# Optimization experiments

Measured on AMD Instinct MI355X. Metric: run time of the kernel, lower is better.

The kernel has to match this reference:

```python
import jax, jax.numpy as jnp
import numpy as np

N, F, E = 50000, 128, 800000
H, C1, C2 = 4, 32, 32  # heads, channel_in, channel_out
LRELU_SLOPE = 0.2
LN_EPS = 1e-5


def _gat_conv(x, src, dst, W_src, W_dst, att_src, att_dst, bias, n, h, c):
    # x: [n, f_in]; src/dst: [e] edge endpoints (message j->i)
    xs = (x @ W_src).reshape(n, h, c)  # source-side transform
    xd = (x @ W_dst).reshape(n, h, c)  # dest-side transform
    a_s = jnp.einsum('nhc,hc->nh', xs, att_src)  # [n,h]
    a_d = jnp.einsum('nhc,hc->nh', xd, att_dst)
    e = jax.nn.leaky_relu(a_s[src] + a_d[dst], LRELU_SLOPE)  # [E,h]
    m = jax.lax.stop_gradient(jax.ops.segment_max(e, dst, num_segments=n))
    ee = jnp.exp(e - m[dst])
    denom = jax.ops.segment_sum(ee, dst, num_segments=n)
    alpha = ee / (denom[dst] + 1e-16)  # segment softmax over incoming edges
    out = jax.ops.segment_sum(xs[src] * alpha[:, :, None], dst, num_segments=n)
    return out.reshape(n, h * c) + bias


def _layer_norm(x, gamma, beta):
    mu = jnp.mean(x, axis=-1, keepdims=True)
    var = jnp.var(x, axis=-1, keepdims=True)
    return (x - mu) * jax.lax.rsqrt(var + LN_EPS) * gamma + beta


def setup_inputs() -> dict:
    key = jax.random.key(0)
    ks = jax.random.split(key, 16)
    hid = H * C1  # 128
    out_dim = H * C2  # 128

    def glorot(k, shape, fan_in):
        return jax.random.normal(k, shape, dtype=jnp.float32) / np.sqrt(fan_in)

    x = jax.random.normal(ks[0], (N, F), dtype=jnp.float32)
    edge_index = jax.random.randint(ks[1], (2, E), 0, N, dtype=jnp.int32)

    return {
        'x': x,
        'edge_index': edge_index,
        # conv1 (in F -> H*C1)
        'W1_src': glorot(ks[2], (F, H * C1), F),
        'W1_dst': glorot(ks[3], (F, H * C1), F),
        'att1_src': glorot(ks[4], (H, C1), C1),
        'att1_dst': glorot(ks[5], (H, C1), C1),
        'b1': jnp.zeros((H * C1,), jnp.float32),
        # lin1 skip (F -> hid)
        'Wl1': glorot(ks[6], (F, hid), F),
        'bl1': jnp.zeros((hid,), jnp.float32),
        # LayerNorm over hid
        'gamma': jnp.ones((hid,), jnp.float32),
        'beta': jnp.zeros((hid,), jnp.float32),
        # conv2 (hid -> H*C2)
        'W2_src': glorot(ks[7], (hid, H * C2), hid),
        'W2_dst': glorot(ks[8], (hid, H * C2), hid),
        'att2_src': glorot(ks[9], (H, C2), C2),
        'att2_dst': glorot(ks[10], (H, C2), C2),
        'b2': jnp.zeros((H * C2,), jnp.float32),
        # lin2 skip (hid -> out_dim)
        'Wl2': glorot(ks[11], (hid, out_dim), hid),
        'bl2': jnp.zeros((out_dim,), jnp.float32),
    }


def reference(x, edge_index, W1_src, W1_dst, att1_src, att1_dst, b1, Wl1, bl1,
              gamma, beta, W2_src, W2_dst, att2_src, att2_dst, b2, Wl2, bl2):
    src, dst = edge_index[0], edge_index[1]
    h = _gat_conv(x, src, dst, W1_src, W1_dst, att1_src, att1_dst, b1, N, H, C1) \
        + (x @ Wl1 + bl1)
    h = jax.nn.relu(_layer_norm(h, gamma, beta))
    out = _gat_conv(h, src, dst, W2_src, W2_dst, att2_src, att2_dst, b2, N, H, C2) \
        + (h @ Wl2 + bl2)
    return out
```

## Files before the change

### kernel.cpp

```cpp
#include <hip/hip_runtime.h>

#define N_NODES 50000
#define E_EDGES 800000
#define LRELU 0.2f
#define LN_EPS 1e-5f
#define NBUCK 196
#define BSHIFT 8
#define BCAP 4608

typedef short bf16x8 __attribute__((ext_vector_type(8)));
typedef float f32x4 __attribute__((ext_vector_type(4)));

__device__ __forceinline__ ushort f2bf(float f) {
    uint u = __float_as_uint(f);
    u += 0x7FFF + ((u >> 16) & 1);
    return (ushort)(u >> 16);
}
__device__ __forceinline__ float bflo(uint u) { return __uint_as_float(u << 16); }
__device__ __forceinline__ float bfhi(uint u) { return __uint_as_float(u & 0xFFFF0000u); }

__global__ __launch_bounds__(256) void bucket_scatter_kernel(
    const int* __restrict__ src, const int* __restrict__ dst,
    int* __restrict__ bucketCursor, uint* __restrict__ pairs, int e)
{
    __shared__ int lhist[256];
    __shared__ int lscan[NBUCK];
    __shared__ int lcur[NBUCK];
    __shared__ int lbase[NBUCK];
    __shared__ uint stageW[4096];
    __shared__ int  stageA[4096];
    int t = threadIdx.x;
    int e0 = blockIdx.x * 4096;
    int count = min(4096, e - e0);

    lhist[t] = 0;
    if (t < NBUCK) lcur[t] = 0;
    __syncthreads();

    int  bb[16];
    uint pk[16];
    #pragma unroll
    for (int q = 0; q < 16; ++q) {
        int li = t + q * 256;
        if (li < count) {
            int d = dst[e0 + li];
            int s = src[e0 + li];
            bb[q] = d >> BSHIFT;
            pk[q] = (uint)s | ((uint)(d & 255) << 16);
            atomicAdd(&lhist[bb[q]], 1);
        } else bb[q] = -1;
    }
    __syncthreads();

    int orig = lhist[t];
    #pragma unroll
    for (int off = 1; off < 256; off <<= 1) {
        int u = (t >= off) ? lhist[t - off] : 0;
        __syncthreads();
        lhist[t] += u;
        __syncthreads();
    }
    if (t < NBUCK) {
        lscan[t] = lhist[t] - orig;
        lbase[t] = t * BCAP + (orig ? atomicAdd(&bucketCursor[t], orig) : 0);
    }
    __syncthreads();

    #pragma unroll
    for (int q = 0; q < 16; ++q) {
        if (bb[q] >= 0) {
            int slot = lscan[bb[q]] + atomicAdd(&lcur[bb[q]], 1);
            stageW[slot] = pk[q];
            stageA[slot] = lbase[bb[q]] + (slot - lscan[bb[q]]);
        }
    }
    __syncthreads();

    #pragma unroll
    for (int q = 0; q < 16; ++q) {
        int li = t + q * 256;
        if (li < count) pairs[stageA[li]] = stageW[li];
    }
}

__global__ __launch_bounds__(256) void bucket_sort_kernel(
    const uint* __restrict__ pairs, const int* __restrict__ bucketCursor,
    int* __restrict__ offs, ushort* __restrict__ degs,
    ushort* __restrict__ srcSorted, int n)
{
    __shared__ int cnt[256], cur[256], ls[256];
    int b = blockIdx.x, t = threadIdx.x;
    int base = b * BCAP;
    int m = bucketCursor[b];
    cnt[t] = 0; cur[t] = 0;
    __syncthreads();
    for (int i = t; i < m; i += 256)
        atomicAdd(&cnt[pairs[base + i] >> 16], 1);
    __syncthreads();
    int orig = cnt[t];
    ls[t] = orig;
    __syncthreads();
    #pragma unroll
    for (int off = 1; off < 256; off <<= 1) {
        int u = (t >= off) ? ls[t - off] : 0;
        __syncthreads();
        ls[t] += u;
        __syncthreads();
    }
    int excl = ls[t] - orig;
    int node = (b << BSHIFT) + t;
    if (node < n) {
        offs[node] = base + excl;
        degs[node] = (ushort)orig;
    }
    cnt[t] = excl;
    __syncthreads();
    for (int i = t; i < m; i += 256) {
        uint w = pairs[base + i];
        int dl = w >> 16;
        int pos = cnt[dl] + atomicAdd(&cur[dl], 1);
        srcSorted[base + pos] = (ushort)(w & 0xFFFFu);
    }
}

__global__ __launch_bounds__(256) void prep_all_kernel(
    const float* __restrict__ W1s, const float* __restrict__ Wl1,
    const float* __restrict__ W1d, const float* __restrict__ a1s,
    const float* __restrict__ a1d,
    const float* __restrict__ W2s, const float* __restrict__ Wl2,
    const float* __restrict__ W2d, const float* __restrict__ a2s,
    const float* __restrict__ a2d,
    ushort* __restrict__ Wt, ushort* __restrict__ Watt,
    int* __restrict__ bucketCursor)
{
    int t = threadIdx.x;
    if (blockIdx.x < 256) {
        int idx = blockIdx.x * 256 + t;
        int lw = idx >> 14, rem = idx & 16383;
        int nn = rem >> 7, k = rem & 127;
        const float* W = (lw == 0) ? W1s : (lw == 1) ? Wl1 : (lw == 2) ? W2s : Wl2;
        Wt[idx] = f2bf(W[k * 128 + nn]);
    } else if (blockIdx.x < 258) {
        int L = blockIdx.x - 256;
        const float* Ws = L ? W2s : W1s;
        const float* Wd = L ? W2d : W1d;
        const float* as = L ? a2s : a1s;
        const float* adv = L ? a2d : a1d;
        #pragma unroll
        for (int q = 0; q < 8; ++q) {
            int e = q * 256 + t;
            int c = e >> 7, f = e & 127;
            float v = 0.f;
            if (c < 8) {
                const float* W  = (c < 4) ? Ws : Wd;
                const float* av = (c < 4) ? as : adv;
                int h = c & 3;
                #pragma unroll
                for (int j = 0; j < 32; ++j)
                    v += W[f * 128 + h * 32 + j] * av[h * 32 + j];
            }
            Watt[L * 2048 + c * 128 + f] = f2bf(v);
        }
    } else {
        if (t < NBUCK) bucketCursor[t] = 0;
    }
}

template <int LAYER>
__global__ __launch_bounds__(256) void gemm_fused_kernel(
    const float* __restrict__ Afp, const ushort* __restrict__ Abf,
    const ushort* __restrict__ Wt, const ushort* __restrict__ Watt,
    ushort* __restrict__ Cbf, float* __restrict__ a_sd, int n)
{
    __shared__ ushort Asb[64][136];
    __shared__ ushort Wsb[128][136];
    __shared__ ushort Attb[16][136];
    const int z = blockIdx.x;
    const int row0 = blockIdx.y * 64;
    const int tid = threadIdx.x;

    if (LAYER == 0) {
        #pragma unroll
        for (int i = 0; i < 8; ++i) {
            int idx = tid + i * 256;
            int r = idx >> 5, c4 = idx & 31;
            int grow = row0 + r;
            float4 v = make_float4(0.f, 0.f, 0.f, 0.f);
            if (grow < n) v = *(const float4*)(Afp + (size_t)grow * 128 + c4 * 4);
            ushort4 o;
            o.x = f2bf(v.x); o.y = f2bf(v.y); o.z = f2bf(v.z); o.w = f2bf(v.w);
            *(ushort4*)&Asb[r][c4 * 4] = o;
        }
    } else {
        #pragma unroll
        for (int i = 0; i < 4; ++i) {
            int c = tid + i * 256;
            int r = c >> 4, o = c & 15;
            int grow = row0 + r;
            uint4 v = make_uint4(0, 0, 0, 0);
            if (grow < n) v = *(const uint4*)(Abf + (size_t)grow * 128 + o * 8);
            *(uint4*)&Asb[r][o * 8] = v;
        }
    }
    {
        const ushort* Wz = Wt + (size_t)(LAYER * 2 + z) * 16384;
        #pragma unroll
        for (int i = 0; i < 8; ++i) {
            int c = tid + i * 256;
            int r = c >> 4, o = c & 15;
            uint4 v = *(const uint4*)(Wz + r * 128 + o * 8);
            *(uint4*)&Wsb[r][o * 8] = v;
        }
    }
    if (z == 0) {
        int r = tid >> 4, o = tid & 15;
        uint4 v = *(const uint4*)(Watt + LAYER * 2048 + r * 128 + o * 8);
        *(uint4*)&Attb[r][o * 8] = v;
    }
    __syncthreads();

    const int w = tid >> 6, lane = tid & 63;
    const int wm = w >> 1, wn = w & 1;
    const int l15 = lane & 15, lg = lane >> 4;
    const bool doAtt = (z == 0) && (wn == 0);

    f32x4 acc[2][4];
    f32x4 accA[2];
    #pragma unroll
    for (int m = 0; m < 2; ++m) {
        accA[m] = (f32x4){0.f, 0.f, 0.f, 0.f};
        #pragma unroll
        for (int j = 0; j < 4; ++j)
            acc[m][j] = (f32x4){0.f, 0.f, 0.f, 0.f};
    }

    #pragma unroll
    for (int ks = 0; ks < 4; ++ks) {
        const int k0 = ks * 32 + 4 * lg;
        bf16x8 af[2], bfr[4];
        #pragma unroll
        for (int m = 0; m < 2; ++m) {
            const ushort* p = &Asb[wm * 32 + m * 16 + l15][k0];
            ushort4 lo = *(const ushort4*)p;
            ushort4 hi = *(const ushort4*)(p + 16);
            bf16x8 a;
            a[0] = (short)lo.x; a[1] = (short)lo.y; a[2] = (short)lo.z; a[3] = (short)lo.w;
            a[4] = (short)hi.x; a[5] = (short)hi.y; a[6] = (short)hi.z; a[7] = (short)hi.w;
            af[m] = a;
        }
        #pragma unroll
        for (int j = 0; j < 4; ++j) {
            const ushort* p = &Wsb[wn * 64 + j * 16 + l15][k0];
            ushort4 lo = *(const ushort4*)p;
            ushort4 hi = *(const ushort4*)(p + 16);
            bf16x8 b;
            b[0] = (short)lo.x; b[1] = (short)lo.y; b[2] = (short)lo.z; b[3] = (short)lo.w;
            b[4] = (short)hi.x; b[5] = (short)hi.y; b[6] = (short)hi.z; b[7] = (short)hi.w;
            bfr[j] = b;
        }
        #pragma unroll
        for (int m = 0; m < 2; ++m)
            #pragma unroll
            for (int j = 0; j < 4; ++j)
                acc[m][j] = __builtin_amdgcn_mfma_f32_16x16x32_bf16(
                    af[m], bfr[j], acc[m][j], 0, 0, 0);
        if (doAtt) {
            const ushort* p = &Attb[l15][k0];
            ushort4 lo = *(const ushort4*)p;
            ushort4 hi = *(const ushort4*)(p + 16);
            bf16x8 b;
            b[0] = (short)lo.x; b[1] = (short)lo.y; b[2] = (short)lo.z; b[3] = (short)lo.w;
            b[4] = (short)hi.x; b[5] = (short)hi.y; b[6] = (short)hi.z; b[7] = (short)hi.w;
            #pragma unroll
            for (int m = 0; m < 2; ++m)
                accA[m] = __builtin_amdgcn_mfma_f32_16x16x32_bf16(
                    af[m], b, accA[m], 0, 0, 0);
        }
    }

    if (doAtt && l15 < 8) {
        #pragma unroll
        for (int m = 0; m < 2; ++m)
            #pragma unroll
            for (int r = 0; r < 4; ++r) {
                int grow = row0 + wm * 32 + m * 16 + lg * 4 + r;
                if (grow < n) a_sd[(size_t)grow * 8 + l15] = accA[m][r];
            }
    }

    __syncthreads();
    ushort (*Cs)[136] = (ushort(*)[136])&Asb[0][0];
    #pragma unroll
    for (int m = 0; m < 2; ++m)
        #pragma unroll
        for (int j = 0; j < 4; ++j)
            #pragma unroll
            for (int r = 0; r < 4; ++r)
                Cs[wm * 32 + m * 16 + lg * 4 + r][wn * 64 + j * 16 + l15] =
                    f2bf(acc[m][j][r]);
    __syncthreads();
    #pragma unroll
    for (int i = 0; i < 4; ++i) {
        int u4 = tid + i * 256;
        int r = u4 >> 4, c8 = u4 & 15;
        int grow = row0 + r;
        if (grow < n) {
            uint4 v = *(const uint4*)&Cs[r][c8 * 8];
            *(uint4*)(Cbf + (size_t)grow * 256 + z * 128 + c8 * 8) = v;
        }
    }
}

template <int MODE>
__global__ __launch_bounds__(256) void aggregate_fused_kernel(
    const ushort* __restrict__ srcSorted, const int* __restrict__ offs,
    const ushort* __restrict__ degs,
    const ushort* __restrict__ bufbf,
    const float* __restrict__ a_sd,
    const float* __restrict__ bias_a, const float* __restrict__ bias_l,
    const float* __restrict__ gamma, const float* __restrict__ beta,
    ushort* __restrict__ hbf, float* __restrict__ out, int n)
{
    int node = (blockIdx.x * blockDim.x + threadIdx.x) >> 6;
    int lane = threadIdx.x & 63;
    if (node >= n) return;
    int beg = offs[node];
    int end = beg + degs[node];
    const int q  = lane & 15;
    const int hh = lane >> 4;
    const int g  = lane & 15;
    const int j  = lane >> 4;
    const int h  = g >> 2;

    float adh = a_sd[(size_t)node * 8 + 4 + hh];

    float acc[8] = {};
    float denp = 0.f;

    for (int t = beg; t < end; t += 16) {
        int idx = t + q;
        int ic = (idx < end) ? idx : (end - 1);
        int s = srcSorted[ic];
        float as = a_sd[(size_t)s * 8 + hh];
        float e = as + adh;
        e = (e > 0.f) ? e : LRELU * e;
        float ee = (idx < end) ? __expf(e) : 0.f;
        denp += ee;

        int   sA  = __shfl(s, j);
        int   sB  = __shfl(s, j + 4);
        int   sC  = __shfl(s, j + 8);
        int   sD  = __shfl(s, j + 12);
        float eeA = __shfl(ee, h * 16 + j);
        float eeB = __shfl(ee, h * 16 + j + 4);
        float eeC = __shfl(ee, h * 16 + j + 8);
        float eeD = __shfl(ee, h * 16 + j + 12);
        uint4 xA = *(const uint4*)(bufbf + (size_t)sA * 256 + g * 8);
        uint4 xB = *(const uint4*)(bufbf + (size_t)sB * 256 + g * 8);
        uint4 xC = *(const uint4*)(bufbf + (size_t)sC * 256 + g * 8);
        uint4 xD = *(const uint4*)(bufbf + (size_t)sD * 256 + g * 8);
        acc[0] = fmaf(eeA, bflo(xA.x), acc[0]);
        acc[1] = fmaf(eeA, bfhi(xA.x), acc[1]);
        acc[2] = fmaf(eeA, bflo(xA.y), acc[2]);
        acc[3] = fmaf(eeA, bfhi(xA.y), acc[3]);
        acc[4] = fmaf(eeA, bflo(xA.z), acc[4]);
        acc[5] = fmaf(eeA, bfhi(xA.z), acc[5]);
        acc[6] = fmaf(eeA, bflo(xA.w), acc[6]);
        acc[7] = fmaf(eeA, bfhi(xA.w), acc[7]);
        acc[0] = fmaf(eeB, bflo(xB.x), acc[0]);
        acc[1] = fmaf(eeB, bfhi(xB.x), acc[1]);
        acc[2] = fmaf(eeB, bflo(xB.y), acc[2]);
        acc[3] = fmaf(eeB, bfhi(xB.y), acc[3]);
        acc[4] = fmaf(eeB, bflo(xB.z), acc[4]);
        acc[5] = fmaf(eeB, bfhi(xB.z), acc[5]);
        acc[6] = fmaf(eeB, bflo(xB.w), acc[6]);
        acc[7] = fmaf(eeB, bfhi(xB.w), acc[7]);
        acc[0] = fmaf(eeC, bflo(xC.x), acc[0]);
        acc[1] = fmaf(eeC, bfhi(xC.x), acc[1]);
        acc[2] = fmaf(eeC, bflo(xC.y), acc[2]);
        acc[3] = fmaf(eeC, bfhi(xC.y), acc[3]);
        acc[4] = fmaf(eeC, bflo(xC.z), acc[4]);
        acc[5] = fmaf(eeC, bfhi(xC.z), acc[5]);
        acc[6] = fmaf(eeC, bflo(xC.w), acc[6]);
        acc[7] = fmaf(eeC, bfhi(xC.w), acc[7]);
        acc[0] = fmaf(eeD, bflo(xD.x), acc[0]);
        acc[1] = fmaf(eeD, bfhi(xD.x), acc[1]);
        acc[2] = fmaf(eeD, bflo(xD.y), acc[2]);
        acc[3] = fmaf(eeD, bfhi(xD.y), acc[3]);
        acc[4] = fmaf(eeD, bflo(xD.z), acc[4]);
        acc[5] = fmaf(eeD, bfhi(xD.z), acc[5]);
        acc[6] = fmaf(eeD, bflo(xD.w), acc[6]);
        acc[7] = fmaf(eeD, bfhi(xD.w), acc[7]);
    }

    #pragma unroll
    for (int c = 0; c < 8; ++c) {
        acc[c] += __shfl_xor(acc[c], 16);
        acc[c] += __shfl_xor(acc[c], 32);
    }
    denp += __shfl_xor(denp, 1);
    denp += __shfl_xor(denp, 2);
    denp += __shfl_xor(denp, 4);
    denp += __shfl_xor(denp, 8);
    float den = __shfl(denp, h * 16);

    if (lane < 16) {
        float inv = 1.f / (den + 1e-16f);
        uint4 sk = *(const uint4*)(bufbf + (size_t)node * 256 + 128 + g * 8);
        float4 ba0 = *(const float4*)(bias_a + g * 8);
        float4 ba1 = *(const float4*)(bias_a + g * 8 + 4);
        float4 bl0 = *(const float4*)(bias_l + g * 8);
        float4 bl1 = *(const float4*)(bias_l + g * 8 + 4);
        float v[8];
        v[0] = acc[0] * inv + bflo(sk.x) + ba0.x + bl0.x;
        v[1] = acc[1] * inv + bfhi(sk.x) + ba0.y + bl0.y;
        v[2] = acc[2] * inv + bflo(sk.y) + ba0.z + bl0.z;
        v[3] = acc[3] * inv + bfhi(sk.y) + ba0.w + bl0.w;
        v[4] = acc[4] * inv + bflo(sk.z) + ba1.x + bl1.x;
        v[5] = acc[5] * inv + bfhi(sk.z) + ba1.y + bl1.y;
        v[6] = acc[6] * inv + bflo(sk.w) + ba1.z + bl1.z;
        v[7] = acc[7] * inv + bfhi(sk.w) + ba1.w + bl1.w;

        if (MODE == 0) {
            float sum = 0.f, sq = 0.f;
            #pragma unroll
            for (int c = 0; c < 8; ++c) { sum += v[c]; sq += v[c] * v[c]; }
            #pragma unroll
            for (int off = 1; off < 16; off <<= 1) {
                sum += __shfl_xor(sum, off);
                sq  += __shfl_xor(sq, off);
            }
            float mu = sum * (1.f / 128.f);
            float var = sq * (1.f / 128.f) - mu * mu;
            float rs = rsqrtf(var + LN_EPS);
            float4 gm0 = *(const float4*)(gamma + g * 8);
            float4 gm1 = *(const float4*)(gamma + g * 8 + 4);
            float4 bt0 = *(const float4*)(beta + g * 8);
            float4 bt1 = *(const float4*)(beta + g * 8 + 4);
            float o[8];
            o[0] = fmaxf((v[0] - mu) * rs * gm0.x + bt0.x, 0.f);
            o[1] = fmaxf((v[1] - mu) * rs * gm0.y + bt0.y, 0.f);
            o[2] = fmaxf((v[2] - mu) * rs * gm0.z + bt0.z, 0.f);
            o[3] = fmaxf((v[3] - mu) * rs * gm0.w + bt0.w, 0.f);
            o[4] = fmaxf((v[4] - mu) * rs * gm1.x + bt1.x, 0.f);
            o[5] = fmaxf((v[5] - mu) * rs * gm1.y + bt1.y, 0.f);
            o[6] = fmaxf((v[6] - mu) * rs * gm1.z + bt1.z, 0.f);
            o[7] = fmaxf((v[7] - mu) * rs * gm1.w + bt1.w, 0.f);
            uint4 st;
            st.x = (uint)f2bf(o[0]) | ((uint)f2bf(o[1]) << 16);
            st.y = (uint)f2bf(o[2]) | ((uint)f2bf(o[3]) << 16);
            st.z = (uint)f2bf(o[4]) | ((uint)f2bf(o[5]) << 16);
            st.w = (uint)f2bf(o[6]) | ((uint)f2bf(o[7]) << 16);
            *(uint4*)(hbf + (size_t)node * 128 + g * 8) = st;
        } else {
            *(float4*)(out + (size_t)node * 128 + g * 8) =
                make_float4(v[0], v[1], v[2], v[3]);
            *(float4*)(out + (size_t)node * 128 + g * 8 + 4) =
                make_float4(v[4], v[5], v[6], v[7]);
        }
    }
}

extern "C" void kernel_launch(void* const* d_in, const int* in_sizes, int n_in,
                              void* d_out, int out_size, void* d_ws, size_t ws_size,
                              hipStream_t stream) {
    const float* x       = (const float*)d_in[0];
    const int*   ei      = (const int*)d_in[1];
    const int*   src     = ei;
    const int*   dst     = ei + E_EDGES;
    const float* W1_src  = (const float*)d_in[2];
    const float* W1_dst  = (const float*)d_in[3];
    const float* att1_s  = (const float*)d_in[4];
    const float* att1_d  = (const float*)d_in[5];
    const float* b1      = (const float*)d_in[6];
    const float* Wl1     = (const float*)d_in[7];
    const float* bl1     = (const float*)d_in[8];
    const float* gamma   = (const float*)d_in[9];
    const float* beta    = (const float*)d_in[10];
    const float* W2_src  = (const float*)d_in[11];
    const float* W2_dst  = (const float*)d_in[12];
    const float* att2_s  = (const float*)d_in[13];
    const float* att2_d  = (const float*)d_in[14];
    const float* b2      = (const float*)d_in[15];
    const float* Wl2     = (const float*)d_in[16];
    const float* bl2     = (const float*)d_in[17];
    float* out = (float*)d_out;

    char* p = (char*)d_ws;
    float* a_sd        = (float*)p;      p += (size_t)N_NODES * 8 * 4;
    int* offs          = (int*)p;        p += (size_t)N_NODES * 4;
    int* bucketCursor  = (int*)p;        p += 256 * 4;
    uint* pairs        = (uint*)p;       p += (size_t)NBUCK * BCAP * 4;
    ushort* degs       = (ushort*)p;     p += (size_t)N_NODES * 2;
    ushort* hbf        = (ushort*)p;     p += (size_t)N_NODES * 128 * 2;
    ushort* bufbf      = (ushort*)p;     p += (size_t)N_NODES * 256 * 2;
    ushort* Wt         = (ushort*)p;     p += (size_t)4 * 16384 * 2;
    ushort* Watt       = (ushort*)p;     p += (size_t)2 * 2048 * 2;
    ushort* srcSorted  = (ushort*)p;     p += (size_t)NBUCK * BCAP * 2;

    dim3 ggrid(2, (N_NODES + 63) / 64);
    int edge_blocks = (E_EDGES + 4095) / 4096;
    int wave_grid   = (N_NODES + 3) / 4;

    prep_all_kernel<<<259, 256, 0, stream>>>(
        W1_src, Wl1, W1_dst, att1_s, att1_d,
        W2_src, Wl2, W2_dst, att2_s, att2_d, Wt, Watt, bucketCursor);
    bucket_scatter_kernel<<<edge_blocks, 256, 0, stream>>>(src, dst, bucketCursor, pairs, E_EDGES);
    bucket_sort_kernel<<<NBUCK, 256, 0, stream>>>(pairs, bucketCursor, offs, degs, srcSorted, N_NODES);

    gemm_fused_kernel<0><<<ggrid, 256, 0, stream>>>(x, nullptr, Wt, Watt, bufbf, a_sd, N_NODES);
    aggregate_fused_kernel<0><<<wave_grid, 256, 0, stream>>>(
        srcSorted, offs, degs, bufbf, a_sd, b1, bl1, gamma, beta, hbf, nullptr, N_NODES);

    gemm_fused_kernel<1><<<ggrid, 256, 0, stream>>>(nullptr, hbf, Wt, Watt, bufbf, a_sd, N_NODES);
    aggregate_fused_kernel<1><<<wave_grid, 256, 0, stream>>>(
        srcSorted, offs, degs, bufbf, a_sd, b2, bl2, nullptr, nullptr, nullptr, out, N_NODES);
}
```

Before: 287.7 us.

## Load source indices per lane in GAT aggregation; use wave-shuffle scans in bucket sort

The aggregation loop is remapped so each lane reads its own four source indices from srcSorted and issues the feature gathers right away. Before, the gathers had to wait on index shuffles. Attention logits are now computed with a head-by-edge-group lane layout, so only the four exp weights are shuffled, and the denominator reduction is changed to match. The two bucket-sort kernels replace their 8-step shared-memory Hillis-Steele scans, each step needing two barriers, with a wave-level shuffle scan plus a small cross-wave fixup. Each lane now issues redundant srcSorted loads, and the new index mapping has to be exactly right to stay correct.

```diff
diff --git a/kernel.cpp b/kernel.cpp
--- a/kernel.cpp
+++ b/kernel.cpp
@@ -27,6 +27,7 @@
     __shared__ int lscan[NBUCK];
     __shared__ int lcur[NBUCK];
     __shared__ int lbase[NBUCK];
+    __shared__ int wsum[4];
     __shared__ uint stageW[4096];
     __shared__ int  stageA[4096];
     int t = threadIdx.x;
@@ -53,15 +54,20 @@
     __syncthreads();
 
     int orig = lhist[t];
-    #pragma unroll
-    for (int off = 1; off < 256; off <<= 1) {
-        int u = (t >= off) ? lhist[t - off] : 0;
-        __syncthreads();
-        lhist[t] += u;
-        __syncthreads();
-    }
+    int lane64 = t & 63, wv = t >> 6;
+    int incl = orig;
+    #pragma unroll
+    for (int off = 1; off < 64; off <<= 1) {
+        int u = __shfl_up(incl, off);
+        if (lane64 >= off) incl += u;
+    }
+    if (lane64 == 63) wsum[wv] = incl;
+    __syncthreads();
+    if (wv > 0) incl += wsum[0];
+    if (wv > 1) incl += wsum[1];
+    if (wv > 2) incl += wsum[2];
     if (t < NBUCK) {
-        lscan[t] = lhist[t] - orig;
+        lscan[t] = incl - orig;
         lbase[t] = t * BCAP + (orig ? atomicAdd(&bucketCursor[t], orig) : 0);
     }
     __syncthreads();
@@ -88,7 +94,8 @@
     int* __restrict__ offs, ushort* __restrict__ degs,
     ushort* __restrict__ srcSorted, int n)
 {
-    __shared__ int cnt[256], cur[256], ls[256];
+    __shared__ int cnt[256], cur[256];
+    __shared__ int wsum[4];
     int b = blockIdx.x, t = threadIdx.x;
     int base = b * BCAP;
     int m = bucketCursor[b];
@@ -97,17 +104,22 @@
     for (int i = t; i < m; i += 256)
         atomicAdd(&cnt[pairs[base + i] >> 16], 1);
     __syncthreads();
+
     int orig = cnt[t];
-    ls[t] = orig;
-    __syncthreads();
-    #pragma unroll
-    for (int off = 1; off < 256; off <<= 1) {
-        int u = (t >= off) ? ls[t - off] : 0;
-        __syncthreads();
-        ls[t] += u;
-        __syncthreads();
-    }
-    int excl = ls[t] - orig;
+    int lane64 = t & 63, wv = t >> 6;
+    int incl = orig;
+    #pragma unroll
+    for (int off = 1; off < 64; off <<= 1) {
+        int u = __shfl_up(incl, off);
+        if (lane64 >= off) incl += u;
+    }
+    if (lane64 == 63) wsum[wv] = incl;
+    __syncthreads();
+    if (wv > 0) incl += wsum[0];
+    if (wv > 1) incl += wsum[1];
+    if (wv > 2) incl += wsum[2];
+    int excl = incl - orig;
+
     int node = (b << BSHIFT) + t;
     if (node < n) {
         offs[node] = base + excl;
@@ -326,71 +338,73 @@
     if (node >= n) return;
     int beg = offs[node];
     int end = beg + degs[node];
-    const int q  = lane & 15;
-    const int hh = lane >> 4;
-    const int g  = lane & 15;
-    const int j  = lane >> 4;
-    const int h  = g >> 2;
-
-    float adh = a_sd[(size_t)node * 8 + 4 + hh];
+    const int j = lane >> 4;
+    const int g = lane & 15;
+    const int a = (lane >> 2) & 3;
+    const int b = lane & 3;
+    const int h = g >> 2;
+
+    float ada = a_sd[(size_t)node * 8 + 4 + a];
 
     float acc[8] = {};
     float denp = 0.f;
 
     for (int t = beg; t < end; t += 16) {
-        int idx = t + q;
-        int ic = (idx < end) ? idx : (end - 1);
-        int s = srcSorted[ic];
-        float as = a_sd[(size_t)s * 8 + hh];
-        float e = as + adh;
+        int i0 = t + j;
+        int i1 = t + j + 4;
+        int i2 = t + j + 8;
+        int i3 = t + j + 12;
+        int s0 = srcSorted[(i0 < end) ? i0 : (end - 1)];
+        int s1 = srcSorted[(i1 < end) ? i1 : (end - 1)];
+        int s2 = srcSorted[(i2 < end) ? i2 : (end - 1)];
+        int s3 = srcSorted[(i3 < end) ? i3 : (end - 1)];
+        uint4 x0 = *(const uint4*)(bufbf + (size_t)s0 * 256 + g * 8);
+        uint4 x1 = *(const uint4*)(bufbf + (size_t)s1 * 256 + g * 8);
+        uint4 x2 = *(const uint4*)(bufbf + (size_t)s2 * 256 + g * 8);
+        uint4 x3 = *(const uint4*)(bufbf + (size_t)s3 * 256 + g * 8);
+        int se = (b == 0) ? s0 : (b == 1) ? s1 : (b == 2) ? s2 : s3;
+        int ie = t + j + 4 * b;
+        float as = a_sd[(size_t)se * 8 + a];
+        float e = as + ada;
         e = (e > 0.f) ? e : LRELU * e;
-        float ee = (idx < end) ? __expf(e) : 0.f;
+        float ee = (ie < end) ? __expf(e) : 0.f;
         denp += ee;
-
-        int   sA  = __shfl(s, j);
-        int   sB  = __shfl(s, j + 4);
-        int   sC  = __shfl(s, j + 8);
-        int   sD  = __shfl(s, j + 12);
-        float eeA = __shfl(ee, h * 16 + j);
-        float eeB = __shfl(ee, h * 16 + j + 4);
-        float eeC = __shfl(ee, h * 16 + j + 8);
-        float eeD = __shfl(ee, h * 16 + j + 12);
-        uint4 xA = *(const uint4*)(bufbf + (size_t)sA * 256 + g * 8);
-        uint4 xB = *(const uint4*)(bufbf + (size_t)sB * 256 + g * 8);
-        uint4 xC = *(const uint4*)(bufbf + (size_t)sC * 256 + g * 8);
-        uint4 xD = *(const uint4*)(bufbf + (size_t)sD * 256 + g * 8);
-        acc[0] = fmaf(eeA, bflo(xA.x), acc[0]);
-        acc[1] = fmaf(eeA, bfhi(xA.x), acc[1]);
-        acc[2] = fmaf(eeA, bflo(xA.y), acc[2]);
-        acc[3] = fmaf(eeA, bfhi(xA.y), acc[3]);
-        acc[4] = fmaf(eeA, bflo(xA.z), acc[4]);
-        acc[5] = fmaf(eeA, bfhi(xA.z), acc[5]);
-        acc[6] = fmaf(eeA, bflo(xA.w), acc[6]);
-        acc[7] = fmaf(eeA, bfhi(xA.w), acc[7]);
-        acc[0] = fmaf(eeB, bflo(xB.x), acc[0]);
-        acc[1] = fmaf(eeB, bfhi(xB.x), acc[1]);
-        acc[2] = fmaf(eeB, bflo(xB.y), acc[2]);
-        acc[3] = fmaf(eeB, bfhi(xB.y), acc[3]);
-        acc[4] = fmaf(eeB, bflo(xB.z), acc[4]);
-        acc[5] = fmaf(eeB, bfhi(xB.z), acc[5]);
-        acc[6] = fmaf(eeB, bflo(xB.w), acc[6]);
-        acc[7] = fmaf(eeB, bfhi(xB.w), acc[7]);
-        acc[0] = fmaf(eeC, bflo(xC.x), acc[0]);
-        acc[1] = fmaf(eeC, bfhi(xC.x), acc[1]);
-        acc[2] = fmaf(eeC, bflo(xC.y), acc[2]);
-        acc[3] = fmaf(eeC, bfhi(xC.y), acc[3]);
-        acc[4] = fmaf(eeC, bflo(xC.z), acc[4]);
-        acc[5] = fmaf(eeC, bfhi(xC.z), acc[5]);
-        acc[6] = fmaf(eeC, bflo(xC.w), acc[6]);
-        acc[7] = fmaf(eeC, bfhi(xC.w), acc[7]);
-        acc[0] = fmaf(eeD, bflo(xD.x), acc[0]);
-        acc[1] = fmaf(eeD, bfhi(xD.x), acc[1]);
-        acc[2] = fmaf(eeD, bflo(xD.y), acc[2]);
-        acc[3] = fmaf(eeD, bfhi(xD.y), acc[3]);
-        acc[4] = fmaf(eeD, bflo(xD.z), acc[4]);
-        acc[5] = fmaf(eeD, bfhi(xD.z), acc[5]);
-        acc[6] = fmaf(eeD, bflo(xD.w), acc[6]);
-        acc[7] = fmaf(eeD, bfhi(xD.w), acc[7]);
+        float ee0 = __shfl(ee, 16 * j + 4 * h + 0);
+        float ee1 = __shfl(ee, 16 * j + 4 * h + 1);
+        float ee2 = __shfl(ee, 16 * j + 4 * h + 2);
+        float ee3 = __shfl(ee, 16 * j + 4 * h + 3);
+        acc[0] = fmaf(ee0, bflo(x0.x), acc[0]);
+        acc[1] = fmaf(ee0, bfhi(x0.x), acc[1]);
+        acc[2] = fmaf(ee0, bflo(x0.y), acc[2]);
+        acc[3] = fmaf(ee0, bfhi(x0.y), acc[3]);
+        acc[4] = fmaf(ee0, bflo(x0.z), acc[4]);
+        acc[5] = fmaf(ee0, bfhi(x0.z), acc[5]);
+        acc[6] = fmaf(ee0, bflo(x0.w), acc[6]);
+        acc[7] = fmaf(ee0, bfhi(x0.w), acc[7]);
+        acc[0] = fmaf(ee1, bflo(x1.x), acc[0]);
+        acc[1] = fmaf(ee1, bfhi(x1.x), acc[1]);
+        acc[2] = fmaf(ee1, bflo(x1.y), acc[2]);
+        acc[3] = fmaf(ee1, bfhi(x1.y), acc[3]);
+        acc[4] = fmaf(ee1, bflo(x1.z), acc[4]);
+        acc[5] = fmaf(ee1, bfhi(x1.z), acc[5]);
+        acc[6] = fmaf(ee1, bflo(x1.w), acc[6]);
+        acc[7] = fmaf(ee1, bfhi(x1.w), acc[7]);
+        acc[0] = fmaf(ee2, bflo(x2.x), acc[0]);
+        acc[1] = fmaf(ee2, bfhi(x2.x), acc[1]);
+        acc[2] = fmaf(ee2, bflo(x2.y), acc[2]);
+        acc[3] = fmaf(ee2, bfhi(x2.y), acc[3]);
+        acc[4] = fmaf(ee2, bflo(x2.z), acc[4]);
+        acc[5] = fmaf(ee2, bfhi(x2.z), acc[5]);
+        acc[6] = fmaf(ee2, bflo(x2.w), acc[6]);
+        acc[7] = fmaf(ee2, bfhi(x2.w), acc[7]);
+        acc[0] = fmaf(ee3, bflo(x3.x), acc[0]);
+        acc[1] = fmaf(ee3, bfhi(x3.x), acc[1]);
+        acc[2] = fmaf(ee3, bflo(x3.y), acc[2]);
+        acc[3] = fmaf(ee3, bfhi(x3.y), acc[3]);
+        acc[4] = fmaf(ee3, bflo(x3.z), acc[4]);
+        acc[5] = fmaf(ee3, bfhi(x3.z), acc[5]);
+        acc[6] = fmaf(ee3, bflo(x3.w), acc[6]);
+        acc[7] = fmaf(ee3, bfhi(x3.w), acc[7]);
     }
 
     #pragma unroll
@@ -400,9 +414,9 @@
     }
     denp += __shfl_xor(denp, 1);
     denp += __shfl_xor(denp, 2);
-    denp += __shfl_xor(denp, 4);
-    denp += __shfl_xor(denp, 8);
-    float den = __shfl(denp, h * 16);
+    denp += __shfl_xor(denp, 16);
+    denp += __shfl_xor(denp, 32);
+    float den = denp;
 
     if (lane < 16) {
         float inv = 1.f / (den + 1e-16f);
```

New measurement: 282.4 us. About the same (-1.8%).
